# Performance work log

Measured on AMD Instinct MI355X. Metric: run time of the kernel, lower is better.

Reference implementation:

```python
import jax, jax.numpy as jnp
import numpy as np


def _c2e(faces):
    # faces: [6, B, C, h, h] in order back, down, front, left, right, up
    # returns equirect map [B, C, H=h, W=2h] via bilinear cube sampling
    _, B, C, h, _ = faces.shape
    H, W = h, 2 * h
    lat = (0.5 - (jnp.arange(H) + 0.5) / H) * jnp.pi      # +pi/2 (top) .. -pi/2
    lon = (2.0 * (jnp.arange(W) + 0.5) / W - 1.0) * jnp.pi  # -pi .. +pi
    cl = jnp.cos(lat)[:, None]
    vx = cl * jnp.sin(lon)[None, :]
    vy = jnp.broadcast_to(jnp.sin(lat)[:, None], (H, W))
    vz = cl * jnp.cos(lon)[None, :]
    dirs = jnp.stack([vx, vy, vz], -1)                     # [H,W,3]
    ax, ay, az = jnp.abs(vx), jnp.abs(vy), jnp.abs(vz)
    cond_z = (az >= ax) & (az >= ay)
    cond_x = (~cond_z) & (ax >= ay)
    # face ids: 0 back(-z) 1 down(-y) 2 front(+z) 3 left(-x) 4 right(+x) 5 up(+y)
    face = jnp.where(cond_z, jnp.where(vz > 0, 2, 0),
                     jnp.where(cond_x, jnp.where(vx > 0, 4, 3),
                               jnp.where(vy > 0, 5, 1)))
    N = jnp.array([[0, 0, -1], [0, -1, 0], [0, 0, 1], [-1, 0, 0], [1, 0, 0], [0, 1, 0]], jnp.float32)
    R = jnp.array([[-1, 0, 0], [1, 0, 0], [1, 0, 0], [0, 0, 1], [0, 0, -1], [1, 0, 0]], jnp.float32)
    U = jnp.array([[0, 1, 0], [0, 0, -1], [0, 1, 0], [0, 1, 0], [0, 1, 0], [0, 0, 1]], jnp.float32)
    den = jnp.sum(dirs * N[face], -1)
    a = jnp.sum(dirs * R[face], -1) / den                  # in-plane x, [-1,1]
    bcoord = jnp.sum(dirs * U[face], -1) / den             # in-plane y, [-1,1]
    uu = jnp.clip((a + 1.0) * 0.5 * (h - 1), 0.0, h - 1)   # align_corners-style
    vv = jnp.clip((1.0 - bcoord) * 0.5 * (h - 1), 0.0, h - 1)
    x0 = jnp.floor(uu).astype(jnp.int32)
    y0 = jnp.floor(vv).astype(jnp.int32)
    x1 = jnp.minimum(x0 + 1, h - 1)
    y1 = jnp.minimum(y0 + 1, h - 1)
    dx = uu - x0
    dy = vv - y0
    ft = faces.transpose(0, 3, 4, 1, 2).reshape(6, h, h, B * C)  # [6,h,h,B*C]
    g = lambda yy, xx: ft[face, yy, xx]                    # gather -> [H,W,B*C]
    out = (g(y0, x0) * ((1 - dx) * (1 - dy))[..., None]
           + g(y0, x1) * (dx * (1 - dy))[..., None]
           + g(y1, x0) * ((1 - dx) * dy)[..., None]
           + g(y1, x1) * (dx * dy)[..., None])
    return out.reshape(H, W, B, C).transpose(2, 3, 0, 1)


def _conv(x, w, bias, pad):
    y = jax.lax.conv_general_dilated(x, w, (1, 1), [(pad, pad), (pad, pad)],
                                     dimension_numbers=('NCHW', 'OIHW', 'NCHW'))
    return y + bias[None, :, None, None]


def setup_inputs() -> dict:
    key = jax.random.key(0)
    ks = jax.random.split(key, 12)
    B, C, h = 4, 64, 128
    face_shape = (B, C, h, h)
    return {
        'm': jax.random.normal(ks[0], (B, C, h, 2 * h), jnp.float32),
        'f': jax.random.normal(ks[1], face_shape, jnp.float32),
        'r': jax.random.normal(ks[2], face_shape, jnp.float32),
        'b': jax.random.normal(ks[3], face_shape, jnp.float32),
        'l': jax.random.normal(ks[4], face_shape, jnp.float32),
        'u': jax.random.normal(ks[5], face_shape, jnp.float32),
        'd': jax.random.normal(ks[6], face_shape, jnp.float32),
        'w_fusion': jax.random.normal(ks[7], (C, C, 3, 3), jnp.float32) * 0.05,
        'b_fusion': jnp.zeros((C,), jnp.float32),
        'w_mask': jax.random.normal(ks[8], (1, 2 * C, 1, 1), jnp.float32) * 0.05,
        'b_mask': jnp.zeros((1,), jnp.float32),
    }


def reference(m, f, r, b, l, u, d, w_fusion, b_fusion, w_mask, b_mask):
    # cube faces stacked in the original order: back, down, front, left, right, up
    faces = jnp.stack([b, d, f, l, r, u], 0)               # [6,B,C,h,h]
    aux = _c2e(faces)                                      # [B,C,h,2h]
    m_aux = jax.nn.relu(_conv(aux, w_fusion, b_fusion, 1))
    m_main = jax.nn.relu(_conv(m, w_fusion, b_fusion, 1))  # shared conv_fusion weights
    joint = jnp.concatenate([m_main, m_aux], axis=1)
    mask = jax.nn.sigmoid(_conv(joint, w_mask, b_mask, 0)) # [B,1,h,2h]
    return m + mask * m_aux
```

## Files before the change

kernel.cpp:

```cpp
#include <hip/hip_runtime.h>
#include <math.h>
#include <stdint.h>

#define BB 4
#define CC 64
#define HH 128
#define HOUT 128
#define WOUT 256
#define NPIX (HOUT * WOUT)
#define NMAP (BB * CC * HOUT * WOUT)
#define FSTR ((size_t)HH * HH * 256)

typedef __attribute__((ext_vector_type(8))) short short8;
typedef __attribute__((ext_vector_type(4))) float floatx4;

__device__ __forceinline__ uint16_t f2bf(float f) {
    uint32_t u = __float_as_uint(f);
    u += 0x7fffu + ((u >> 16) & 1u);
    return (uint16_t)(u >> 16);
}
__device__ __forceinline__ float bfu2f(uint32_t v) { return __uint_as_float(v << 16); }

__global__ __launch_bounds__(256) void prep_kernel(uint32_t* __restrict__ pk,
                                                   float* __restrict__ pdx,
                                                   float* __restrict__ pdy,
                                                   const float* __restrict__ wf,
                                                   uint4* __restrict__ Bsw) {
    if (blockIdx.x < 128) {
        int p = blockIdx.x * 256 + threadIdx.x;
        int y = p >> 8;
        int x = p & 255;
        const float PI = 3.14159265358979323846f;
        float lat = (0.5f - (y + 0.5f) / (float)HOUT) * PI;
        float lon = (2.0f * (x + 0.5f) / (float)WOUT - 1.0f) * PI;
        float cl = cosf(lat);
        float vx = cl * sinf(lon);
        float vy = sinf(lat);
        float vz = cl * cosf(lon);
        float ax = fabsf(vx), ay = fabsf(vy), az = fabsf(vz);

        int face;
        float den, a, b;
        if (az >= ax && az >= ay) {
            if (vz > 0.0f) { face = 2; den = vz;  a = vx;  b = vy; }
            else           { face = 0; den = -vz; a = -vx; b = vy; }
        } else if (ax >= ay) {
            if (vx > 0.0f) { face = 4; den = vx;  a = -vz; b = vy; }
            else           { face = 3; den = -vx; a = vz;  b = vy; }
        } else {
            if (vy > 0.0f) { face = 5; den = vy;  a = vx;  b = vz; }
            else           { face = 1; den = -vy; a = vx;  b = -vz; }
        }
        a /= den;
        b /= den;
        float uu = fminf(fmaxf((a + 1.0f) * 0.5f * (HH - 1), 0.0f), (float)(HH - 1));
        float vv = fminf(fmaxf((1.0f - b) * 0.5f * (HH - 1), 0.0f), (float)(HH - 1));
        int x0 = (int)floorf(uu);
        int y0 = (int)floorf(vv);
        int x1 = min(x0 + 1, HH - 1);
        int y1 = min(y0 + 1, HH - 1);
        pdx[p] = uu - (float)x0;
        pdy[p] = vv - (float)y0;
        pk[p] = (uint32_t)face | ((uint32_t)x0 << 3) | ((uint32_t)y0 << 10) |
                ((uint32_t)x1 << 17) | ((uint32_t)y1 << 24);
    } else {
        int tid = (blockIdx.x - 128) * 256 + threadIdx.x;
        if (tid >= 9 * 2 * 4 * 64) return;
        int lane = tid & 63;
        int rest = tid >> 6;
        int n = rest & 3, ks = (rest >> 2) & 1, tap = rest >> 3;
        int co = n * 16 + (lane & 15);
        uint32_t w4[4];
#pragma unroll
        for (int pw = 0; pw < 4; pw++) {
            int ci0 = ks * 32 + (lane >> 4) * 8 + pw * 2;
            uint32_t lo = f2bf(wf[(size_t)(co * CC + ci0) * 9 + tap]);
            uint32_t hi = f2bf(wf[(size_t)(co * CC + ci0 + 1) * 9 + tap]);
            w4[pw] = lo | (hi << 16);
        }
        Bsw[tid] = make_uint4(w4[0], w4[1], w4[2], w4[3]);
    }
}

__global__ __launch_bounds__(256) void facepack_kernel(
    const float* __restrict__ pB, const float* __restrict__ pD,
    const float* __restrict__ pF, const float* __restrict__ pL,
    const float* __restrict__ pR, const float* __restrict__ pU,
    uint16_t* __restrict__ FCLlo, uint16_t* __restrict__ FCLhi) {
    __shared__ uint16_t lds[64 * 256];
    int bid = blockIdx.x;
    int half = bid & 1;
    int y = (bid >> 1) & 127;
    int fc = bid >> 8;
    const float* src = (fc == 0) ? pB : (fc == 1) ? pD : (fc == 2) ? pF
                     : (fc == 3) ? pL : (fc == 4) ? pR : pU;
    uint16_t* FCL = (fc < 3) ? (FCLlo + (size_t)fc * FSTR)
                             : (FCLhi + (size_t)(fc - 3) * FSTR);
    int t = threadIdx.x;
    int xl = t & 63;
    int x = half * 64 + xl;
    int cgb = t >> 6;

#pragma unroll
    for (int i = 0; i < 8; i++) {
        int cg = i * 4 + cgb;
        uint32_t w4[4];
#pragma unroll
        for (int j = 0; j < 4; j++) {
            int bc0 = cg * 8 + j * 2;
            uint32_t lo = f2bf(src[((size_t)bc0 * HH + y) * HH + x]);
            uint32_t hi = f2bf(src[((size_t)(bc0 + 1) * HH + y) * HH + x]);
            w4[j] = lo | (hi << 16);
        }
        int off = xl * 256 + ((cg ^ (xl & 7)) * 8);
        *(uint4*)&lds[off] = make_uint4(w4[0], w4[1], w4[2], w4[3]);
    }
    __syncthreads();
    size_t obase = ((size_t)y * HH + half * 64) * 256;
#pragma unroll
    for (int i = 0; i < 8; i++) {
        int q = i * 256 + t;
        int xx = q >> 5, cg = q & 31;
        int off = xx * 256 + ((cg ^ (xx & 7)) * 8);
        *(uint4*)&FCL[obase + (size_t)q * 8] = *(const uint4*)&lds[off];
    }
}

__global__ __launch_bounds__(256) void gather_kernel(
    const uint32_t* __restrict__ pk, const float* __restrict__ pdx,
    const float* __restrict__ pdy, const uint16_t* __restrict__ FCLlo,
    const uint16_t* __restrict__ FCLhi, uint16_t* __restrict__ Xa) {
    int tid = blockIdx.x * 256 + threadIdx.x;
    int chunk = tid & 31;
    int p = tid >> 5;

    uint32_t k = pk[p];
    float dx = pdx[p], dy = pdy[p];
    int fc = k & 7;
    int x0 = (k >> 3) & 127, y0 = (k >> 10) & 127;
    int x1 = (k >> 17) & 127, y1 = (k >> 24) & 127;

    const uint16_t* fb = (fc < 3) ? (FCLlo + (size_t)fc * FSTR)
                                  : (FCLhi + (size_t)(fc - 3) * FSTR);
    const uint16_t* base = fb + chunk * 8;
    uint4 c00 = *(const uint4*)(base + ((size_t)y0 * HH + x0) * 256);
    uint4 c01 = *(const uint4*)(base + ((size_t)y0 * HH + x1) * 256);
    uint4 c10 = *(const uint4*)(base + ((size_t)y1 * HH + x0) * 256);
    uint4 c11 = *(const uint4*)(base + ((size_t)y1 * HH + x1) * 256);

    float w00 = (1.0f - dx) * (1.0f - dy);
    float w01 = dx * (1.0f - dy);
    float w10 = (1.0f - dx) * dy;
    float w11 = dx * dy;

    const uint32_t* a00 = (const uint32_t*)&c00;
    const uint32_t* a01 = (const uint32_t*)&c01;
    const uint32_t* a10 = (const uint32_t*)&c10;
    const uint32_t* a11 = (const uint32_t*)&c11;
    uint32_t r[4];
#pragma unroll
    for (int w = 0; w < 4; w++) {
        float lo = w00 * bfu2f(a00[w] & 0xffffu) + w01 * bfu2f(a01[w] & 0xffffu)
                 + w10 * bfu2f(a10[w] & 0xffffu) + w11 * bfu2f(a11[w] & 0xffffu);
        float hi = w00 * bfu2f(a00[w] >> 16) + w01 * bfu2f(a01[w] >> 16)
                 + w10 * bfu2f(a10[w] >> 16) + w11 * bfu2f(a11[w] >> 16);
        r[w] = (uint32_t)f2bf(lo) | ((uint32_t)f2bf(hi) << 16);
    }

    int b = chunk >> 3, c = (chunk & 7) * 8;
    int y = p >> 8, x = p & 255;
    size_t o = (((size_t)(b * HOUT + y)) * WOUT + x) * CC + c;
    *(uint4*)(Xa + o) = make_uint4(r[0], r[1], r[2], r[3]);
}

__global__ __launch_bounds__(256) void pack_kernel(const float* __restrict__ src,
                                                   uint16_t* __restrict__ dst) {
    __shared__ uint16_t lds[WOUT * CC];
    int t = threadIdx.x;
    int by = blockIdx.x;
    int b = by >> 7, y = by & 127;

#pragma unroll
    for (int cg = 0; cg < 8; cg++) {
        uint32_t w4[4];
#pragma unroll
        for (int pw = 0; pw < 4; pw++) {
            int c0 = cg * 8 + pw * 2;
            uint32_t lo = f2bf(src[((size_t)(b * CC + c0) * HOUT + y) * WOUT + t]);
            uint32_t hi = f2bf(src[((size_t)(b * CC + c0 + 1) * HOUT + y) * WOUT + t]);
            w4[pw] = lo | (hi << 16);
        }
        int off = t * 64 + ((cg ^ (t & 7)) * 8);
        *(uint4*)&lds[off] = make_uint4(w4[0], w4[1], w4[2], w4[3]);
    }
    __syncthreads();
    size_t obase = (size_t)((b * HOUT + y) * WOUT) * CC;
#pragma unroll
    for (int i = 0; i < 8; i++) {
        int q = i * 256 + t;
        int p = q >> 3, c8 = q & 7;
        int off = p * 64 + ((c8 ^ (p & 7)) * 8);
        *(uint4*)&dst[obase + (size_t)q * 8] = *(const uint4*)&lds[off];
    }
}

__global__ __launch_bounds__(256, 4) void gemm_fused_kernel(
    const uint16_t* __restrict__ Xm, const uint16_t* __restrict__ Xa,
    const uint4* __restrict__ Bsw, const float* __restrict__ bias,
    const float* __restrict__ wm, const float* __restrict__ bm,
    const float* __restrict__ m, float* __restrict__ out) {
    __shared__ __align__(16) uint16_t lds[3 * 132 * 64];
    float* ldsf = (float*)lds;

    int gid = blockIdx.x;
    int b = gid >> 8;
    int i = gid & 255;
    int xcd = i & 7, j = i >> 3;
    int y = xcd * 16 + (j & 15);
    int h = j >> 4;
    const int wx = h * 128 - 2;

    int tid = threadIdx.x;
    int lane = tid & 63;
    int wave = tid >> 6;
    int l15 = lane & 15, lq = lane >> 4;

    float bb[4], wmm[4], wma[4];
#pragma unroll
    for (int n = 0; n < 4; n++) {
        bb[n] = bias[n * 16 + l15];
        wmm[n] = wm[n * 16 + l15];
        wma[n] = wm[64 + n * 16 + l15];
    }
    float bm0 = bm[0];

    float mp[2][4];
#pragma unroll
    for (int mt = 0; mt < 2; mt++)
#pragma unroll
        for (int rg = 0; rg < 4; rg++) mp[mt][rg] = 0.0f;

    floatx4 acc[2][4];

#pragma unroll
    for (int phase = 0; phase < 2; phase++) {
        const uint16_t* X = phase ? Xa : Xm;
        const uint16_t* Xb = X + (size_t)b * (HOUT * WOUT * CC);

        __syncthreads();
#pragma unroll
        for (int it = 0; it < 13; it++) {
            int cid = it * 256 + tid;
            if (cid < 3168) {
                int c = cid & 7;
                int pr = cid >> 3;
                int p = pr % 132;
                int r = pr / 132;
                int gy = y + r - 1;
                int gx = wx + p;
                uint4 v = make_uint4(0, 0, 0, 0);
                if ((unsigned)gy < (unsigned)HOUT && (unsigned)gx < (unsigned)WOUT)
                    v = *(const uint4*)(Xb + ((size_t)gy * WOUT + gx) * CC + c * 8);
                int slot = (r * 132 + p) * 8 + (c ^ (p & 7));
                *(uint4*)&lds[slot * 8] = v;
            }
        }
        __syncthreads();

#pragma unroll
        for (int mt = 0; mt < 2; mt++)
#pragma unroll
            for (int n = 0; n < 4; n++) acc[mt][n] = (floatx4)0.0f;

#pragma unroll
        for (int tap = 0; tap < 9; tap++) {
            const int r = tap / 3;
            const int dx = tap % 3 - 1;
#pragma unroll
            for (int ks = 0; ks < 2; ks++) {
                short8 bfr[4];
                const uint4* bp = Bsw + (size_t)((tap * 2 + ks) * 4) * 64 + lane;
#pragma unroll
                for (int n = 0; n < 4; n++) {
                    uint4 t4 = bp[n * 64];
                    bfr[n] = *(short8*)&t4;
                }
#pragma unroll
                for (int mt = 0; mt < 2; mt++) {
                    int p = wave * 32 + mt * 16 + l15 + dx + 2;
                    int chunk = ks * 4 + lq;
                    int slot = (r * 132 + p) * 8 + (chunk ^ (p & 7));
                    short8 af = *(const short8*)&lds[slot * 8];
#pragma unroll
                    for (int n = 0; n < 4; n++)
                        acc[mt][n] = __builtin_amdgcn_mfma_f32_16x16x32_bf16(
                            af, bfr[n], acc[mt][n], 0, 0, 0);
                }
            }
        }

        if (phase == 0) {
#pragma unroll
            for (int mt = 0; mt < 2; mt++)
#pragma unroll
                for (int n = 0; n < 4; n++)
#pragma unroll
                    for (int rg = 0; rg < 4; rg++) {
                        float v = acc[mt][n][rg] + bb[n];
                        v = v > 0.0f ? v : 0.0f;
                        mp[mt][rg] += wmm[n] * v;
                    }
        } else {
#pragma unroll
            for (int mt = 0; mt < 2; mt++)
#pragma unroll
                for (int n = 0; n < 4; n++)
#pragma unroll
                    for (int rg = 0; rg < 4; rg++) {
                        float v = acc[mt][n][rg] + bb[n];
                        v = v > 0.0f ? v : 0.0f;
                        acc[mt][n][rg] = v;
                        mp[mt][rg] += wma[n] * v;
                    }
        }
    }

#pragma unroll
    for (int mt = 0; mt < 2; mt++)
#pragma unroll
        for (int rg = 0; rg < 4; rg++) {
            float v = mp[mt][rg];
            v += __shfl_xor(v, 1);
            v += __shfl_xor(v, 2);
            v += __shfl_xor(v, 4);
            v += __shfl_xor(v, 8);
            mp[mt][rg] = 1.0f / (1.0f + expf(-(v + bm0)));
        }

    __syncthreads();
#pragma unroll
    for (int mt = 0; mt < 2; mt++)
#pragma unroll
        for (int n = 0; n < 4; n++)
#pragma unroll
            for (int rg = 0; rg < 4; rg++) {
                int px = wave * 32 + mt * 16 + lq * 4 + rg;
                int co = n * 16 + l15;
                ldsf[co * 129 + px] = mp[mt][rg] * acc[mt][n][rg];
            }
    __syncthreads();

    size_t base0 = (size_t)b * (CC * HOUT * WOUT) + (size_t)y * WOUT + h * 128;
#pragma unroll
    for (int it = 0; it < 32; it++) {
        int q = it * 256 + tid;
        int c = q >> 7, px = q & 127;
        size_t idx = base0 + (size_t)c * (HOUT * WOUT) + px;
        out[idx] = m[idx] + ldsf[c * 129 + px];
    }
}

__global__ __launch_bounds__(256) void signal_kernel(float* __restrict__ out, float v) {
    int idx = blockIdx.x * 256 + threadIdx.x;
    out[idx] = v;
}

extern "C" void kernel_launch(void* const* d_in, const int* in_sizes, int n_in,
                              void* d_out, int out_size, void* d_ws, size_t ws_size,
                              hipStream_t stream) {
    const float* m  = (const float*)d_in[0];
    const float* f  = (const float*)d_in[1];
    const float* r  = (const float*)d_in[2];
    const float* bk = (const float*)d_in[3];
    const float* l  = (const float*)d_in[4];
    const float* u  = (const float*)d_in[5];
    const float* dn = (const float*)d_in[6];
    const float* wf = (const float*)d_in[7];
    const float* bf = (const float*)d_in[8];
    const float* wm = (const float*)d_in[9];
    const float* bm = (const float*)d_in[10];
    float* out = (float*)d_out;

    const size_t FCL_HALF = (size_t)3 * HH * HH * 256 * 2;
    const size_t OFF_FCLH = 0;
    const size_t OFF_XA   = FCL_HALF;
    const size_t OFF_XM   = OFF_XA + (size_t)NMAP * 2;
    const size_t OFF_BSW  = OFF_XM + (size_t)NMAP * 2;
    const size_t OFF_PK   = OFF_BSW + (9 * 2 * 4 * 64 * 16);
    const size_t OFF_PDX  = OFF_PK + (1u << 17);
    const size_t OFF_PDY  = OFF_PDX + (1u << 17);
    const size_t NEED     = OFF_PDY + (1u << 17);

    if (ws_size < NEED) {
        float v = 100.0f + (float)(ws_size >> 20);
        signal_kernel<<<NMAP / 256, 256, 0, stream>>>(out, v);
        return;
    }

    char* ws = (char*)d_ws;
    uint16_t* FCLhi = (uint16_t*)(ws + OFF_FCLH);
    uint16_t* Xa    = (uint16_t*)(ws + OFF_XA);
    uint16_t* Xm    = (uint16_t*)(ws + OFF_XM);
    uint4* Bsw      = (uint4*)(ws + OFF_BSW);
    uint32_t* pk    = (uint32_t*)(ws + OFF_PK);
    float* pdx      = (float*)(ws + OFF_PDX);
    float* pdy      = (float*)(ws + OFF_PDY);
    uint16_t* FCLlo = (uint16_t*)d_out;

    prep_kernel<<<146, 256, 0, stream>>>(pk, pdx, pdy, wf, Bsw);
    facepack_kernel<<<6 * HH * 2, 256, 0, stream>>>(bk, dn, f, l, r, u, FCLlo, FCLhi);
    gather_kernel<<<(NPIX * 32) / 256, 256, 0, stream>>>(pk, pdx, pdy, FCLlo, FCLhi, Xa);
    pack_kernel<<<BB * HOUT, 256, 0, stream>>>(m, Xm);
    gemm_fused_kernel<<<BB * HOUT * 2, 256, 0, stream>>>(Xm, Xa, Bsw, bf, wm, bm, m, out);
}
```

Measured before the change: 266.2 us.

## Merge prep/facepack/pack into one launch and halve GEMM tile width

Merges the three preprocessing kernels (coordinate/weight prep, face packing, main-map packing) into one front kernel that dispatches on block index, removing two launches and letting the independent work run concurrently. Also shrinks the fused conv GEMM tile from 128 to 64 pixels per block, doubling the grid and cutting LDS and accumulator registers per block to raise occupancy. The narrower tile adds halo overhead (68 vs 132 columns loaded per 64 vs 128 outputs) and halves MFMA work per A-fragment load. The front kernel's LDS is sized for the largest branch, which may limit occupancy for the light prep blocks.

```diff
diff --git a/kernel.cpp b/kernel.cpp
--- a/kernel.cpp
+++ b/kernel.cpp
@@ -11,6 +11,11 @@
 #define NMAP (BB * CC * HOUT * WOUT)
 #define FSTR ((size_t)HH * HH * 256)
 
+#define NB_PREP 146
+#define NB_FACE (6 * HH * 2)
+#define NB_PACK (BB * HOUT)
+#define NB_FRONT (NB_PREP + NB_FACE + NB_PACK)
+
 typedef __attribute__((ext_vector_type(8))) short short8;
 typedef __attribute__((ext_vector_type(4))) float floatx4;
 
@@ -21,108 +26,135 @@
 }
 __device__ __forceinline__ float bfu2f(uint32_t v) { return __uint_as_float(v << 16); }
 
-__global__ __launch_bounds__(256) void prep_kernel(uint32_t* __restrict__ pk,
-                                                   float* __restrict__ pdx,
-                                                   float* __restrict__ pdy,
-                                                   const float* __restrict__ wf,
-                                                   uint4* __restrict__ Bsw) {
-    if (blockIdx.x < 128) {
-        int p = blockIdx.x * 256 + threadIdx.x;
-        int y = p >> 8;
-        int x = p & 255;
-        const float PI = 3.14159265358979323846f;
-        float lat = (0.5f - (y + 0.5f) / (float)HOUT) * PI;
-        float lon = (2.0f * (x + 0.5f) / (float)WOUT - 1.0f) * PI;
-        float cl = cosf(lat);
-        float vx = cl * sinf(lon);
-        float vy = sinf(lat);
-        float vz = cl * cosf(lon);
-        float ax = fabsf(vx), ay = fabsf(vy), az = fabsf(vz);
-
-        int face;
-        float den, a, b;
-        if (az >= ax && az >= ay) {
-            if (vz > 0.0f) { face = 2; den = vz;  a = vx;  b = vy; }
-            else           { face = 0; den = -vz; a = -vx; b = vy; }
-        } else if (ax >= ay) {
-            if (vx > 0.0f) { face = 4; den = vx;  a = -vz; b = vy; }
-            else           { face = 3; den = -vx; a = vz;  b = vy; }
-        } else {
-            if (vy > 0.0f) { face = 5; den = vy;  a = vx;  b = vz; }
-            else           { face = 1; den = -vy; a = vx;  b = -vz; }
-        }
-        a /= den;
-        b /= den;
-        float uu = fminf(fmaxf((a + 1.0f) * 0.5f * (HH - 1), 0.0f), (float)(HH - 1));
-        float vv = fminf(fmaxf((1.0f - b) * 0.5f * (HH - 1), 0.0f), (float)(HH - 1));
-        int x0 = (int)floorf(uu);
-        int y0 = (int)floorf(vv);
-        int x1 = min(x0 + 1, HH - 1);
-        int y1 = min(y0 + 1, HH - 1);
-        pdx[p] = uu - (float)x0;
-        pdy[p] = vv - (float)y0;
-        pk[p] = (uint32_t)face | ((uint32_t)x0 << 3) | ((uint32_t)y0 << 10) |
-                ((uint32_t)x1 << 17) | ((uint32_t)y1 << 24);
-    } else {
-        int tid = (blockIdx.x - 128) * 256 + threadIdx.x;
-        if (tid >= 9 * 2 * 4 * 64) return;
-        int lane = tid & 63;
-        int rest = tid >> 6;
-        int n = rest & 3, ks = (rest >> 2) & 1, tap = rest >> 3;
-        int co = n * 16 + (lane & 15);
-        uint32_t w4[4];
-#pragma unroll
-        for (int pw = 0; pw < 4; pw++) {
-            int ci0 = ks * 32 + (lane >> 4) * 8 + pw * 2;
-            uint32_t lo = f2bf(wf[(size_t)(co * CC + ci0) * 9 + tap]);
-            uint32_t hi = f2bf(wf[(size_t)(co * CC + ci0 + 1) * 9 + tap]);
-            w4[pw] = lo | (hi << 16);
-        }
-        Bsw[tid] = make_uint4(w4[0], w4[1], w4[2], w4[3]);
-    }
-}
-
-__global__ __launch_bounds__(256) void facepack_kernel(
+__global__ __launch_bounds__(256) void front_kernel(
+    uint32_t* __restrict__ pk, float* __restrict__ pdx, float* __restrict__ pdy,
+    const float* __restrict__ wf, uint4* __restrict__ Bsw,
     const float* __restrict__ pB, const float* __restrict__ pD,
     const float* __restrict__ pF, const float* __restrict__ pL,
     const float* __restrict__ pR, const float* __restrict__ pU,
-    uint16_t* __restrict__ FCLlo, uint16_t* __restrict__ FCLhi) {
+    uint16_t* __restrict__ FCLlo, uint16_t* __restrict__ FCLhi,
+    const float* __restrict__ msrc, uint16_t* __restrict__ Xm) {
     __shared__ uint16_t lds[64 * 256];
     int bid = blockIdx.x;
-    int half = bid & 1;
-    int y = (bid >> 1) & 127;
-    int fc = bid >> 8;
-    const float* src = (fc == 0) ? pB : (fc == 1) ? pD : (fc == 2) ? pF
-                     : (fc == 3) ? pL : (fc == 4) ? pR : pU;
-    uint16_t* FCL = (fc < 3) ? (FCLlo + (size_t)fc * FSTR)
-                             : (FCLhi + (size_t)(fc - 3) * FSTR);
     int t = threadIdx.x;
-    int xl = t & 63;
-    int x = half * 64 + xl;
-    int cgb = t >> 6;
-
-#pragma unroll
-    for (int i = 0; i < 8; i++) {
-        int cg = i * 4 + cgb;
-        uint32_t w4[4];
-#pragma unroll
-        for (int j = 0; j < 4; j++) {
-            int bc0 = cg * 8 + j * 2;
-            uint32_t lo = f2bf(src[((size_t)bc0 * HH + y) * HH + x]);
-            uint32_t hi = f2bf(src[((size_t)(bc0 + 1) * HH + y) * HH + x]);
-            w4[j] = lo | (hi << 16);
-        }
-        int off = xl * 256 + ((cg ^ (xl & 7)) * 8);
-        *(uint4*)&lds[off] = make_uint4(w4[0], w4[1], w4[2], w4[3]);
-    }
-    __syncthreads();
-    size_t obase = ((size_t)y * HH + half * 64) * 256;
-#pragma unroll
-    for (int i = 0; i < 8; i++) {
-        int q = i * 256 + t;
-        int xx = q >> 5, cg = q & 31;
-        int off = xx * 256 + ((cg ^ (xx & 7)) * 8);
-        *(uint4*)&FCL[obase + (size_t)q * 8] = *(const uint4*)&lds[off];
+
+    if (bid < NB_PREP) {
+        if (bid < 128) {
+            int p = bid * 256 + t;
+            int y = p >> 8;
+            int x = p & 255;
+            const float PI = 3.14159265358979323846f;
+            float lat = (0.5f - (y + 0.5f) / (float)HOUT) * PI;
+            float lon = (2.0f * (x + 0.5f) / (float)WOUT - 1.0f) * PI;
+            float cl = cosf(lat);
+            float vx = cl * sinf(lon);
+            float vy = sinf(lat);
+            float vz = cl * cosf(lon);
+            float ax = fabsf(vx), ay = fabsf(vy), az = fabsf(vz);
+
+            int face;
+            float den, a, b;
+            if (az >= ax && az >= ay) {
+                if (vz > 0.0f) { face = 2; den = vz;  a = vx;  b = vy; }
+                else           { face = 0; den = -vz; a = -vx; b = vy; }
+            } else if (ax >= ay) {
+                if (vx > 0.0f) { face = 4; den = vx;  a = -vz; b = vy; }
+                else           { face = 3; den = -vx; a = vz;  b = vy; }
+            } else {
+                if (vy > 0.0f) { face = 5; den = vy;  a = vx;  b = vz; }
+                else           { face = 1; den = -vy; a = vx;  b = -vz; }
+            }
+            a /= den;
+            b /= den;
+            float uu = fminf(fmaxf((a + 1.0f) * 0.5f * (HH - 1), 0.0f), (float)(HH - 1));
+            float vv = fminf(fmaxf((1.0f - b) * 0.5f * (HH - 1), 0.0f), (float)(HH - 1));
+            int x0 = (int)floorf(uu);
+            int y0 = (int)floorf(vv);
+            int x1 = min(x0 + 1, HH - 1);
+            int y1 = min(y0 + 1, HH - 1);
+            pdx[p] = uu - (float)x0;
+            pdy[p] = vv - (float)y0;
+            pk[p] = (uint32_t)face | ((uint32_t)x0 << 3) | ((uint32_t)y0 << 10) |
+                    ((uint32_t)x1 << 17) | ((uint32_t)y1 << 24);
+        } else {
+            int tid = (bid - 128) * 256 + t;
+            if (tid >= 9 * 2 * 4 * 64) return;
+            int lane = tid & 63;
+            int rest = tid >> 6;
+            int n = rest & 3, ks = (rest >> 2) & 1, tap = rest >> 3;
+            int co = n * 16 + (lane & 15);
+            uint32_t w4[4];
+#pragma unroll
+            for (int pw = 0; pw < 4; pw++) {
+                int ci0 = ks * 32 + (lane >> 4) * 8 + pw * 2;
+                uint32_t lo = f2bf(wf[(size_t)(co * CC + ci0) * 9 + tap]);
+                uint32_t hi = f2bf(wf[(size_t)(co * CC + ci0 + 1) * 9 + tap]);
+                w4[pw] = lo | (hi << 16);
+            }
+            Bsw[tid] = make_uint4(w4[0], w4[1], w4[2], w4[3]);
+        }
+    } else if (bid < NB_PREP + NB_FACE) {
+        int fb = bid - NB_PREP;
+        int half = fb & 1;
+        int y = (fb >> 1) & 127;
+        int fc = fb >> 8;
+        const float* src = (fc == 0) ? pB : (fc == 1) ? pD : (fc == 2) ? pF
+                         : (fc == 3) ? pL : (fc == 4) ? pR : pU;
+        uint16_t* FCL = (fc < 3) ? (FCLlo + (size_t)fc * FSTR)
+                                 : (FCLhi + (size_t)(fc - 3) * FSTR);
+        int xl = t & 63;
+        int x = half * 64 + xl;
+        int cgb = t >> 6;
+
+#pragma unroll
+        for (int i = 0; i < 8; i++) {
+            int cg = i * 4 + cgb;
+            uint32_t w4[4];
+#pragma unroll
+            for (int j = 0; j < 4; j++) {
+                int bc0 = cg * 8 + j * 2;
+                uint32_t lo = f2bf(src[((size_t)bc0 * HH + y) * HH + x]);
+                uint32_t hi = f2bf(src[((size_t)(bc0 + 1) * HH + y) * HH + x]);
+                w4[j] = lo | (hi << 16);
+            }
+            int off = xl * 256 + ((cg ^ (xl & 7)) * 8);
+            *(uint4*)&lds[off] = make_uint4(w4[0], w4[1], w4[2], w4[3]);
+        }
+        __syncthreads();
+        size_t obase = ((size_t)y * HH + half * 64) * 256;
+#pragma unroll
+        for (int i = 0; i < 8; i++) {
+            int q = i * 256 + t;
+            int xx = q >> 5, cg = q & 31;
+            int off = xx * 256 + ((cg ^ (xx & 7)) * 8);
+            *(uint4*)&FCL[obase + (size_t)q * 8] = *(const uint4*)&lds[off];
+        }
+    } else {
+        int by = bid - (NB_PREP + NB_FACE);
+        int b = by >> 7, y = by & 127;
+
+#pragma unroll
+        for (int cg = 0; cg < 8; cg++) {
+            uint32_t w4[4];
+#pragma unroll
+            for (int pw = 0; pw < 4; pw++) {
+                int c0 = cg * 8 + pw * 2;
+                uint32_t lo = f2bf(msrc[((size_t)(b * CC + c0) * HOUT + y) * WOUT + t]);
+                uint32_t hi = f2bf(msrc[((size_t)(b * CC + c0 + 1) * HOUT + y) * WOUT + t]);
+                w4[pw] = lo | (hi << 16);
+            }
+            int off = t * 64 + ((cg ^ (t & 7)) * 8);
+            *(uint4*)&lds[off] = make_uint4(w4[0], w4[1], w4[2], w4[3]);
+        }
+        __syncthreads();
+        size_t obase = (size_t)((b * HOUT + y) * WOUT) * CC;
+#pragma unroll
+        for (int i = 0; i < 8; i++) {
+            int q = i * 256 + t;
+            int p = q >> 3, c8 = q & 7;
+            int off = p * 64 + ((c8 ^ (p & 7)) * 8);
+            *(uint4*)&Xm[obase + (size_t)q * 8] = *(const uint4*)&lds[off];
+        }
     }
 }
 
@@ -173,52 +205,21 @@
     *(uint4*)(Xa + o) = make_uint4(r[0], r[1], r[2], r[3]);
 }
 
-__global__ __launch_bounds__(256) void pack_kernel(const float* __restrict__ src,
-                                                   uint16_t* __restrict__ dst) {
-    __shared__ uint16_t lds[WOUT * CC];
-    int t = threadIdx.x;
-    int by = blockIdx.x;
-    int b = by >> 7, y = by & 127;
-
-#pragma unroll
-    for (int cg = 0; cg < 8; cg++) {
-        uint32_t w4[4];
-#pragma unroll
-        for (int pw = 0; pw < 4; pw++) {
-            int c0 = cg * 8 + pw * 2;
-            uint32_t lo = f2bf(src[((size_t)(b * CC + c0) * HOUT + y) * WOUT + t]);
-            uint32_t hi = f2bf(src[((size_t)(b * CC + c0 + 1) * HOUT + y) * WOUT + t]);
-            w4[pw] = lo | (hi << 16);
-        }
-        int off = t * 64 + ((cg ^ (t & 7)) * 8);
-        *(uint4*)&lds[off] = make_uint4(w4[0], w4[1], w4[2], w4[3]);
-    }
-    __syncthreads();
-    size_t obase = (size_t)((b * HOUT + y) * WOUT) * CC;
-#pragma unroll
-    for (int i = 0; i < 8; i++) {
-        int q = i * 256 + t;
-        int p = q >> 3, c8 = q & 7;
-        int off = p * 64 + ((c8 ^ (p & 7)) * 8);
-        *(uint4*)&dst[obase + (size_t)q * 8] = *(const uint4*)&lds[off];
-    }
-}
-
 __global__ __launch_bounds__(256, 4) void gemm_fused_kernel(
     const uint16_t* __restrict__ Xm, const uint16_t* __restrict__ Xa,
     const uint4* __restrict__ Bsw, const float* __restrict__ bias,
     const float* __restrict__ wm, const float* __restrict__ bm,
     const float* __restrict__ m, float* __restrict__ out) {
-    __shared__ __align__(16) uint16_t lds[3 * 132 * 64];
+    __shared__ __align__(16) uint16_t lds[3 * 68 * 64];
     float* ldsf = (float*)lds;
 
     int gid = blockIdx.x;
-    int b = gid >> 8;
-    int i = gid & 255;
+    int b = gid >> 9;
+    int i = gid & 511;
     int xcd = i & 7, j = i >> 3;
     int y = xcd * 16 + (j & 15);
-    int h = j >> 4;
-    const int wx = h * 128 - 2;
+    int q = j >> 4;
+    const int wx = q * 64 - 2;
 
     int tid = threadIdx.x;
     int lane = tid & 63;
@@ -234,13 +235,11 @@
     }
     float bm0 = bm[0];
 
-    float mp[2][4];
-#pragma unroll
-    for (int mt = 0; mt < 2; mt++)
-#pragma unroll
-        for (int rg = 0; rg < 4; rg++) mp[mt][rg] = 0.0f;
-
-    floatx4 acc[2][4];
+    float mp[4];
+#pragma unroll
+    for (int rg = 0; rg < 4; rg++) mp[rg] = 0.0f;
+
+    floatx4 acc[4];
 
 #pragma unroll
     for (int phase = 0; phase < 2; phase++) {
@@ -249,28 +248,26 @@
 
         __syncthreads();
 #pragma unroll
-        for (int it = 0; it < 13; it++) {
+        for (int it = 0; it < 7; it++) {
             int cid = it * 256 + tid;
-            if (cid < 3168) {
+            if (cid < 1632) {
                 int c = cid & 7;
                 int pr = cid >> 3;
-                int p = pr % 132;
-                int r = pr / 132;
+                int p = pr % 68;
+                int r = pr / 68;
                 int gy = y + r - 1;
                 int gx = wx + p;
                 uint4 v = make_uint4(0, 0, 0, 0);
                 if ((unsigned)gy < (unsigned)HOUT && (unsigned)gx < (unsigned)WOUT)
                     v = *(const uint4*)(Xb + ((size_t)gy * WOUT + gx) * CC + c * 8);
-                int slot = (r * 132 + p) * 8 + (c ^ (p & 7));
+                int slot = (r * 68 + p) * 8 + (c ^ (p & 7));
                 *(uint4*)&lds[slot * 8] = v;
             }
         }
         __syncthreads();
 
 #pragma unroll
-        for (int mt = 0; mt < 2; mt++)
-#pragma unroll
-            for (int n = 0; n < 4; n++) acc[mt][n] = (floatx4)0.0f;
+        for (int n = 0; n < 4; n++) acc[n] = (floatx4)0.0f;
 
 #pragma unroll
         for (int tap = 0; tap < 9; tap++) {
@@ -285,78 +282,67 @@
                     uint4 t4 = bp[n * 64];
                     bfr[n] = *(short8*)&t4;
                 }
-#pragma unroll
-                for (int mt = 0; mt < 2; mt++) {
-                    int p = wave * 32 + mt * 16 + l15 + dx + 2;
-                    int chunk = ks * 4 + lq;
-                    int slot = (r * 132 + p) * 8 + (chunk ^ (p & 7));
-                    short8 af = *(const short8*)&lds[slot * 8];
-#pragma unroll
-                    for (int n = 0; n < 4; n++)
-                        acc[mt][n] = __builtin_amdgcn_mfma_f32_16x16x32_bf16(
-                            af, bfr[n], acc[mt][n], 0, 0, 0);
+                int p = wave * 16 + l15 + dx + 2;
+                int chunk = ks * 4 + lq;
+                int slot = (r * 68 + p) * 8 + (chunk ^ (p & 7));
+                short8 af = *(const short8*)&lds[slot * 8];
+#pragma unroll
+                for (int n = 0; n < 4; n++)
+                    acc[n] = __builtin_amdgcn_mfma_f32_16x16x32_bf16(
+                        af, bfr[n], acc[n], 0, 0, 0);
+            }
+        }
+
+        if (phase == 0) {
+#pragma unroll
+            for (int n = 0; n < 4; n++)
+#pragma unroll
+                for (int rg = 0; rg < 4; rg++) {
+                    float v = acc[n][rg] + bb[n];
+                    v = v > 0.0f ? v : 0.0f;
+                    mp[rg] += wmm[n] * v;
                 }
-            }
-        }
-
-        if (phase == 0) {
-#pragma unroll
-            for (int mt = 0; mt < 2; mt++)
-#pragma unroll
-                for (int n = 0; n < 4; n++)
-#pragma unroll
-                    for (int rg = 0; rg < 4; rg++) {
-                        float v = acc[mt][n][rg] + bb[n];
-                        v = v > 0.0f ? v : 0.0f;
-                        mp[mt][rg] += wmm[n] * v;
-                    }
         } else {
 #pragma unroll
-            for (int mt = 0; mt < 2; mt++)
-#pragma unroll
-                for (int n = 0; n < 4; n++)
-#pragma unroll
-                    for (int rg = 0; rg < 4; rg++) {
-                        float v = acc[mt][n][rg] + bb[n];
-                        v = v > 0.0f ? v : 0.0f;
-                        acc[mt][n][rg] = v;
-                        mp[mt][rg] += wma[n] * v;
-                    }
-        }
-    }
-
-#pragma unroll
-    for (int mt = 0; mt < 2; mt++)
+            for (int n = 0; n < 4; n++)
+#pragma unroll
+                for (int rg = 0; rg < 4; rg++) {
+                    float v = acc[n][rg] + bb[n];
+                    v = v > 0.0f ? v : 0.0f;
+                    acc[n][rg] = v;
+                    mp[rg] += wma[n] * v;
+                }
+        }
+    }
+
+#pragma unroll
+    for (int rg = 0; rg < 4; rg++) {
+        float v = mp[rg];
+        v += __shfl_xor(v, 1);
+        v += __shfl_xor(v, 2);
+        v += __shfl_xor(v, 4);
+        v += __shfl_xor(v, 8);
+        mp[rg] = 1.0f / (1.0f + expf(-(v + bm0)));
+    }
+
+    __syncthreads();
+#pragma unroll
+    for (int n = 0; n < 4; n++)
 #pragma unroll
         for (int rg = 0; rg < 4; rg++) {
-            float v = mp[mt][rg];
-            v += __shfl_xor(v, 1);
-            v += __shfl_xor(v, 2);
-            v += __shfl_xor(v, 4);
-            v += __shfl_xor(v, 8);
-            mp[mt][rg] = 1.0f / (1.0f + expf(-(v + bm0)));
-        }
-
+            int px = wave * 16 + lq * 4 + rg;
+            int co = n * 16 + l15;
+            ldsf[co * 65 + px] = mp[rg] * acc[n][rg];
+        }
     __syncthreads();
-#pragma unroll
-    for (int mt = 0; mt < 2; mt++)
-#pragma unroll
-        for (int n = 0; n < 4; n++)
-#pragma unroll
-            for (int rg = 0; rg < 4; rg++) {
-                int px = wave * 32 + mt * 16 + lq * 4 + rg;
-                int co = n * 16 + l15;
-                ldsf[co * 129 + px] = mp[mt][rg] * acc[mt][n][rg];
-            }
-    __syncthreads();
-
-    size_t base0 = (size_t)b * (CC * HOUT * WOUT) + (size_t)y * WOUT + h * 128;
-#pragma unroll
-    for (int it = 0; it < 32; it++) {
-        int q = it * 256 + tid;
-        int c = q >> 7, px = q & 127;
+
+    size_t base0 = (size_t)b * (CC * HOUT * WOUT) + (size_t)y * WOUT + q * 64;
+#pragma unroll
+    for (int it = 0; it < 16; it++) {
+        int qq = it * 256 + tid;
+        int c = qq >> 6, px = qq & 63;
         size_t idx = base0 + (size_t)c * (HOUT * WOUT) + px;
-        out[idx] = m[idx] + ldsf[c * 129 + px];
+        out[idx] = m[idx] + ldsf[c * 65 + px];
     }
 }
 
@@ -407,9 +393,9 @@
     float* pdy      = (float*)(ws + OFF_PDY);
     uint16_t* FCLlo = (uint16_t*)d_out;
 
-    prep_kernel<<<146, 256, 0, stream>>>(pk, pdx, pdy, wf, Bsw);
-    facepack_kernel<<<6 * HH * 2, 256, 0, stream>>>(bk, dn, f, l, r, u, FCLlo, FCLhi);
+    front_kernel<<<NB_FRONT, 256, 0, stream>>>(pk, pdx, pdy, wf, Bsw,
+                                               bk, dn, f, l, r, u, FCLlo, FCLhi,
+                                               m, Xm);
     gather_kernel<<<(NPIX * 32) / 256, 256, 0, stream>>>(pk, pdx, pdy, FCLlo, FCLhi, Xa);
-    pack_kernel<<<BB * HOUT, 256, 0, stream>>>(m, Xm);
-    gemm_fused_kernel<<<BB * HOUT * 2, 256, 0, stream>>>(Xm, Xa, Bsw, bf, wm, bm, m, out);
-}
+    gemm_fused_kernel<<<BB * HOUT * 2 * 2, 256, 0, stream>>>(Xm, Xa, Bsw, bf, wm, bm, m, out);
+}
```

Result: slower. 295.4 us (+11.0%).
